# Performance work log

Hardware: AMD Instinct MI355X
Metric: run time of the kernel (lower is better)

## Reference

```python
import jax, jax.numpy as jnp
import numpy as np

N_NODES = 50000
N_EDGES = 800000
IN_DIM = 128
HID_DIM = 128
OUT_DIM = 128
NUM_GRAPHS = 64
NUM_CLASSES = 3


def _glorot(key, shape):
    lim = np.sqrt(6.0 / (shape[0] + shape[1])).astype(np.float32)
    return jax.random.uniform(key, shape, jnp.float32, -lim, lim)


def setup_inputs() -> dict:
    key = jax.random.key(0)
    ks = jax.random.split(key, 10)
    x = jax.random.normal(ks[0], (N_NODES, IN_DIM), jnp.float32)
    edge_index = jax.random.randint(ks[1], (2, N_EDGES), 0, N_NODES, jnp.int32).astype(jnp.int64)
    batch = jnp.sort(jax.random.randint(ks[2], (N_NODES,), 0, NUM_GRAPHS, jnp.int32)).astype(jnp.int64)
    return {
        "x": x,
        "edge_index": edge_index,
        "batch": batch,
        "W1": _glorot(ks[3], (IN_DIM, HID_DIM)),  "b1": jnp.zeros((HID_DIM,), jnp.float32),
        "W2": _glorot(ks[4], (HID_DIM, HID_DIM)), "b2": jnp.zeros((HID_DIM,), jnp.float32),
        "W3": _glorot(ks[5], (HID_DIM, OUT_DIM)), "b3": jnp.zeros((OUT_DIM,), jnp.float32),
        "C1": _glorot(ks[6], (OUT_DIM, HID_DIM)), "bc1": jnp.zeros((HID_DIM,), jnp.float32),
        "C2": _glorot(ks[7], (HID_DIM, NUM_CLASSES)), "bc2": jnp.zeros((NUM_CLASSES,), jnp.float32),
    }


def _gcn_conv(x, src, dst, norm, W, b):
    # PyG GCNConv: linear transform, then normalized gather/scatter aggregation, then bias.
    h = x @ W                               # [N, F_out]
    msg = h[src] * norm[:, None]            # [E+N, F_out] irregular gather
    return jax.ops.segment_sum(msg, dst, num_segments=N_NODES) + b


def reference(x, edge_index, batch, W1, b1, W2, b2, W3, b3, C1, bc1, C2, bc2):
    loops = jnp.arange(N_NODES, dtype=edge_index.dtype)
    src = jnp.concatenate([edge_index[0], loops])  # add self-loops as in GCNConv
    dst = jnp.concatenate([edge_index[1], loops])
    deg = jax.ops.segment_sum(jnp.ones_like(dst, jnp.float32), dst, num_segments=N_NODES)
    dinv = jnp.where(deg > 0, jax.lax.rsqrt(deg), 0.0)
    norm = dinv[src] * dinv[dst]            # symmetric D^-1/2 (A+I) D^-1/2 weights

    # dropout(p=0.2) is identity at inference time
    h = jax.nn.relu(_gcn_conv(x, src, dst, norm, W1, b1))
    h = jax.nn.relu(_gcn_conv(h, src, dst, norm, W2, b2))
    h = _gcn_conv(h, src, dst, norm, W3, b3)

    # global mean pool over batch segment ids
    counts = jax.ops.segment_sum(jnp.ones((N_NODES,), jnp.float32), batch, num_segments=NUM_GRAPHS)
    pooled = jax.ops.segment_sum(h, batch, num_segments=NUM_GRAPHS) / jnp.maximum(counts, 1.0)[:, None]

    g = jax.nn.relu(pooled @ C1 + bc1)      # classifier MLP (dropout 0.3 inactive)
    return g @ C2 + bc2                     # [NUM_GRAPHS, 3]
```

## Files before the change

kernel.cpp:

```cpp
#include <hip/hip_runtime.h>
#include <hip/hip_bf16.h>

#define N_NODES    50000
#define DIM        128
#define NUM_GRAPHS 64
#define NUM_CLASSES 3
#define NPAD       50176
#define XPITCH     136

typedef unsigned short ushort_t;
typedef unsigned int   uint_t;
typedef __attribute__((ext_vector_type(8))) short short8;
typedef __attribute__((ext_vector_type(4))) float f32x4;

__device__ __forceinline__ ushort_t f2bf(float f) {
    union { float f; uint_t u; } v; v.f = f;
    uint_t r = v.u + 0x7fffu + ((v.u >> 16) & 1u);
    return (ushort_t)(r >> 16);
}
__device__ __forceinline__ float bflo(uint_t u) {
    union { uint_t u; float f; } v; v.u = u << 16; return v.f;
}
__device__ __forceinline__ float bfhi(uint_t u) {
    union { uint_t u; float f; } v; v.u = u & 0xffff0000u; return v.f;
}

__device__ __forceinline__ void accum8(float* a, uint4 u) {
    a[0] += bflo(u.x); a[1] += bfhi(u.x);
    a[2] += bflo(u.y); a[3] += bfhi(u.y);
    a[4] += bflo(u.z); a[5] += bfhi(u.z);
    a[6] += bflo(u.w); a[7] += bfhi(u.w);
}

__device__ __forceinline__ int qsel(int lane, int s0, int s1, int s2, int s3) {
    int lo = (lane & 16) ? s1 : s0;
    int hi = (lane & 16) ? s3 : s2;
    return (lane & 32) ? hi : lo;
}

__device__ __forceinline__ void quad_gather(
    int lane, int m, int myidx0, int p0, int p1,
    const int* __restrict__ csr_src, const uint4* __restrict__ Tb4,
    float* a)
{
    int deg = p1 - p0;
    if (deg < 0) deg = 0;
    int nchunk = (deg + 63) >> 6;
    int myidx = myidx0;
    for (int ck = 0; ck < nchunk; ++ck) {
        int base = p0 + (ck << 6);
        int cnt = p1 - base; if (cnt > 64) cnt = 64;
        int nb = cnt >> 3;
        if (nb > 0) {
            uint4 u0, u1;
            {
                int s = qsel(lane, __builtin_amdgcn_readlane(myidx, 0),
                                   __builtin_amdgcn_readlane(myidx, 1),
                                   __builtin_amdgcn_readlane(myidx, 2),
                                   __builtin_amdgcn_readlane(myidx, 3));
                u0 = Tb4[s * 16 + m];
                s = qsel(lane, __builtin_amdgcn_readlane(myidx, 4),
                               __builtin_amdgcn_readlane(myidx, 5),
                               __builtin_amdgcn_readlane(myidx, 6),
                               __builtin_amdgcn_readlane(myidx, 7));
                u1 = Tb4[s * 16 + m];
            }
            for (int b = 1; b < nb; ++b) {
                int jb = b * 8;
                uint4 n0, n1;
                int s = qsel(lane, __builtin_amdgcn_readlane(myidx, jb),
                                   __builtin_amdgcn_readlane(myidx, jb + 1),
                                   __builtin_amdgcn_readlane(myidx, jb + 2),
                                   __builtin_amdgcn_readlane(myidx, jb + 3));
                n0 = Tb4[s * 16 + m];
                s = qsel(lane, __builtin_amdgcn_readlane(myidx, jb + 4),
                               __builtin_amdgcn_readlane(myidx, jb + 5),
                               __builtin_amdgcn_readlane(myidx, jb + 6),
                               __builtin_amdgcn_readlane(myidx, jb + 7));
                n1 = Tb4[s * 16 + m];
                accum8(a, u0); accum8(a, u1);
                u0 = n0; u1 = n1;
            }
            accum8(a, u0); accum8(a, u1);
        }
        int j = nb * 8;
        for (; j + 4 <= cnt; j += 4) {
            int s = qsel(lane, __builtin_amdgcn_readlane(myidx, j),
                               __builtin_amdgcn_readlane(myidx, j + 1),
                               __builtin_amdgcn_readlane(myidx, j + 2),
                               __builtin_amdgcn_readlane(myidx, j + 3));
            uint4 u = Tb4[s * 16 + m];
            accum8(a, u);
        }
        if (j < cnt) {
            int rem = cnt - j;
            int s0 = __builtin_amdgcn_readlane(myidx, j);
            int s1 = __builtin_amdgcn_readlane(myidx, (j + 1 < cnt) ? j + 1 : j);
            int s2 = __builtin_amdgcn_readlane(myidx, (j + 2 < cnt) ? j + 2 : j);
            int s  = qsel(lane, s0, s1, s2, s0);
            if ((lane >> 4) < rem) {
                uint4 u = Tb4[s * 16 + m];
                accum8(a, u);
            }
        }
        if (ck + 1 < nchunk) {
            int c2 = p1 - (base + 64);
            myidx = (lane < c2) ? csr_src[base + 64 + lane] : 0;
        }
    }
}

__global__ void k_init(int* degi, float* pooled, float* counts) {
    int i = blockIdx.x * 256 + threadIdx.x;
    if (i < NPAD) degi[i] = 0;
    if (i < NUM_GRAPHS * DIM) pooled[i] = 0.0f;
    if (i < NUM_GRAPHS) counts[i] = 0.0f;
}

__global__ void k_prep(const float* __restrict__ W1, const float* __restrict__ W2,
                       const float* __restrict__ W3, ushort_t* __restrict__ Wt) {
    int i = blockIdx.x * 256 + threadIdx.x;
    int mat = i >> 14;
    int idx = i & 16383;
    const float* W = (mat == 0) ? W1 : (mat == 1) ? W2 : W3;
    int n = idx >> 7, k = idx & 127;
    Wt[mat * 16384 + n * 128 + k] = f2bf(W[k * 128 + n]);
}

__global__ void k_count(const int* __restrict__ dst, int* degi, int* rank, int nedges) {
    int e = blockIdx.x * 256 + threadIdx.x;
    if (e < nedges) rank[e] = atomicAdd(&degi[dst[e]], 1);
}

__global__ __launch_bounds__(256) void k_scan1(const int* __restrict__ degi,
                                               int* rowptr, int* bsum) {
    __shared__ int sh[256];
    int i = blockIdx.x * 256 + threadIdx.x;
    int v = degi[i];
    sh[threadIdx.x] = v;
    __syncthreads();
    for (int off = 1; off < 256; off <<= 1) {
        int t = (threadIdx.x >= off) ? sh[threadIdx.x - off] : 0;
        __syncthreads();
        sh[threadIdx.x] += t;
        __syncthreads();
    }
    rowptr[i] = sh[threadIdx.x] - v;
    if (threadIdx.x == 255) bsum[blockIdx.x] = sh[255];
}

__global__ __launch_bounds__(256) void k_scan2(int* bsum, int nblocks) {
    __shared__ int sh[256];
    int v = (threadIdx.x < nblocks) ? bsum[threadIdx.x] : 0;
    sh[threadIdx.x] = v;
    __syncthreads();
    for (int off = 1; off < 256; off <<= 1) {
        int t = (threadIdx.x >= off) ? sh[threadIdx.x - off] : 0;
        __syncthreads();
        sh[threadIdx.x] += t;
        __syncthreads();
    }
    if (threadIdx.x < nblocks) bsum[threadIdx.x] = sh[threadIdx.x] - v;
}

__global__ __launch_bounds__(256) void k_scan3(int* rowptr, const int* __restrict__ bsum,
                                               const int* __restrict__ degi,
                                               float* dinv) {
    int i = blockIdx.x * 256 + threadIdx.x;
    rowptr[i] = rowptr[i] + bsum[blockIdx.x];
    if (i < N_NODES) dinv[i] = rsqrtf((float)degi[i] + 1.0f);
}

__global__ void k_fill(const int* __restrict__ src, const int* __restrict__ dst,
                       const int* __restrict__ rank, const int* __restrict__ rowptr,
                       int* csr_src, int nedges) {
    int e = blockIdx.x * 256 + threadIdx.x;
    if (e < nedges) csr_src[rowptr[dst[e]] + rank[e]] = src[e];
}

__global__ __launch_bounds__(256) void k_mm1(
    const float* __restrict__ xin, const ushort_t* __restrict__ WtG,
    const float* __restrict__ dinv, ushort_t* __restrict__ TbOut)
{
    __shared__ ushort_t Wl[DIM * XPITCH];
    __shared__ ushort_t Xl[64 * XPITCH];

    const int tid = threadIdx.x;
    const int rowbase = blockIdx.x * 64;

    #pragma unroll
    for (int i = 0; i < 8; ++i) {
        int g = tid + i * 256;
        uint4 v = ((const uint4*)WtG)[g];
        *((uint4*)&Wl[(g >> 4) * XPITCH + (g & 15) * 8]) = v;
    }
    #pragma unroll
    for (int i = 0; i < 8; ++i) {
        int c = tid + i * 256;
        int row = c >> 5;
        int grow = rowbase + row;
        float4 f = make_float4(0.f, 0.f, 0.f, 0.f);
        if (grow < N_NODES)
            f = ((const float4*)xin)[(long long)rowbase * 32 + c];
        ushort4 h;
        h.x = f2bf(f.x); h.y = f2bf(f.y); h.z = f2bf(f.z); h.w = f2bf(f.w);
        *((ushort4*)&Xl[row * XPITCH + (c & 31) * 4]) = h;
    }
    __syncthreads();

    const int wave = tid >> 6;
    const int lane = tid & 63;
    const int quad = lane >> 4;
    const int lm   = lane & 15;
    const int m0   = wave * 16;

    short8 af[4];
    #pragma unroll
    for (int k0 = 0; k0 < 4; ++k0)
        af[k0] = *(const short8*)&Xl[(m0 + lm) * XPITCH + k0 * 32 + quad * 8];

    int noder[4]; float di[4]; bool okr[4];
    #pragma unroll
    for (int r = 0; r < 4; ++r) {
        noder[r] = rowbase + m0 + quad * 4 + r;
        okr[r] = (noder[r] < N_NODES);
        di[r] = okr[r] ? dinv[noder[r]] : 0.f;
    }

    for (int n0 = 0; n0 < DIM; n0 += 16) {
        f32x4 acc = {0.f, 0.f, 0.f, 0.f};
        #pragma unroll
        for (int k0 = 0; k0 < 4; ++k0) {
            short8 bf = *(const short8*)&Wl[(n0 + lm) * XPITCH + k0 * 32 + quad * 8];
            acc = __builtin_amdgcn_mfma_f32_16x16x32_bf16(af[k0], bf, acc, 0, 0, 0);
        }
        int n = n0 + lm;
        #pragma unroll
        for (int r = 0; r < 4; ++r)
            if (okr[r])
                TbOut[(long long)noder[r] * DIM + n] = f2bf(acc[r] * di[r]);
    }
}

__global__ __launch_bounds__(256) void k_fused(
    const int* __restrict__ rowptr, const int* __restrict__ csr_src,
    const float* __restrict__ dinv, const uint_t* __restrict__ TbIn,
    const ushort_t* __restrict__ WtG, const float* __restrict__ b_prev,
    ushort_t* __restrict__ TbOut)
{
    __shared__ ushort_t Xl[16 * XPITCH];

    const int tid = threadIdx.x;
    const int rowbase = blockIdx.x * 16;
    const int wave = tid >> 6;
    const int lane = tid & 63;
    const int m    = lane & 15;
    const uint4* Tb4 = (const uint4*)TbIn;

    float4 blo = ((const float4*)b_prev)[m * 2];
    float4 bhi = ((const float4*)b_prev)[m * 2 + 1];

    const int nfirst = rowbase + wave * 4;
    int pv = (lane < 5) ? rowptr[nfirst + lane] : 0;
    int p[5];
    #pragma unroll
    for (int i = 0; i < 5; ++i) p[i] = __builtin_amdgcn_readlane(pv, i);

    int idx_n;
    {
        int d0 = p[1] - p[0];
        idx_n = (lane < d0) ? csr_src[p[0] + lane] : 0;
    }

    #pragma unroll
    for (int t = 0; t < 4; ++t) {
        int idx_cur = idx_n;
        if (t < 3) {
            int dn = p[t + 2] - p[t + 1];
            idx_n = (lane < dn) ? csr_src[p[t + 1] + lane] : 0;
        }
        int r = wave * 4 + t;
        int n = rowbase + r;
        float a[8] = {0.f, 0.f, 0.f, 0.f, 0.f, 0.f, 0.f, 0.f};
        float dd = 0.f;
        uint4 us = make_uint4(0u, 0u, 0u, 0u);
        if (n < N_NODES) {
            us = Tb4[n * 16 + m];
            dd = dinv[n];
            quad_gather(lane, m, idx_cur, p[t], p[t + 1], csr_src, Tb4, a);
        }
        #pragma unroll
        for (int i = 0; i < 8; ++i) {
            a[i] += __shfl_xor(a[i], 16);
            a[i] += __shfl_xor(a[i], 32);
        }
        accum8(a, us);
        if (lane < 16) {
            short8 hh;
            hh[0] = (short)f2bf(fmaxf(blo.x + a[0] * dd, 0.f));
            hh[1] = (short)f2bf(fmaxf(blo.y + a[1] * dd, 0.f));
            hh[2] = (short)f2bf(fmaxf(blo.z + a[2] * dd, 0.f));
            hh[3] = (short)f2bf(fmaxf(blo.w + a[3] * dd, 0.f));
            hh[4] = (short)f2bf(fmaxf(bhi.x + a[4] * dd, 0.f));
            hh[5] = (short)f2bf(fmaxf(bhi.y + a[5] * dd, 0.f));
            hh[6] = (short)f2bf(fmaxf(bhi.z + a[6] * dd, 0.f));
            hh[7] = (short)f2bf(fmaxf(bhi.w + a[7] * dd, 0.f));
            *((short8*)&Xl[r * XPITCH + m * 8]) = hh;
        }
    }
    __syncthreads();

    const int quad = lane >> 4;
    const int lm   = lane & 15;

    short8 af[4];
    #pragma unroll
    for (int k0 = 0; k0 < 4; ++k0)
        af[k0] = *(const short8*)&Xl[lm * XPITCH + k0 * 32 + quad * 8];

    int noder[4]; float di[4]; bool okr[4];
    #pragma unroll
    for (int r = 0; r < 4; ++r) {
        noder[r] = rowbase + quad * 4 + r;
        okr[r] = (noder[r] < N_NODES);
        di[r] = okr[r] ? dinv[noder[r]] : 0.f;
    }

    #pragma unroll
    for (int hh = 0; hh < 2; ++hh) {
        int n0 = wave * 32 + hh * 16;
        f32x4 acc = {0.f, 0.f, 0.f, 0.f};
        #pragma unroll
        for (int k0 = 0; k0 < 4; ++k0) {
            short8 bf = *(const short8*)&WtG[(n0 + lm) * DIM + k0 * 32 + quad * 8];
            acc = __builtin_amdgcn_mfma_f32_16x16x32_bf16(af[k0], bf, acc, 0, 0, 0);
        }
        int n = n0 + lm;
        #pragma unroll
        for (int r = 0; r < 4; ++r)
            if (okr[r])
                TbOut[(long long)noder[r] * DIM + n] = f2bf(acc[r] * di[r]);
    }
}

__global__ __launch_bounds__(256) void k_poolgather(
    const int* __restrict__ rowptr, const int* __restrict__ csr_src,
    const float* __restrict__ dinv, const uint_t* __restrict__ Tb,
    const float* __restrict__ b3, const int* __restrict__ batch,
    float* pooled, float* counts)
{
    __shared__ float lp[8][DIM];
    __shared__ float lc[8];

    const int tid  = threadIdx.x;
    const int wave = tid >> 6;
    const int lane = tid & 63;
    const int m    = lane & 15;
    const int q    = lane >> 4;
    const int blk0 = blockIdx.x * 32;
    const uint4* Tb4 = (const uint4*)Tb;
    const int ch = 8 * m + 2 * q;

    #pragma unroll
    for (int i = 0; i < 4; ++i) ((float*)lp)[tid + i * 256] = 0.f;
    if (tid < 8) lc[tid] = 0.f;
    __syncthreads();

    const int gbase = batch[min(blk0, N_NODES - 1)];
    int n0 = blk0 + wave * 8;

    if (n0 < N_NODES) {
        int nend = min(n0 + 8, N_NODES);
        float bb0 = b3[ch], bb1 = b3[ch + 1];

        int pv = (lane < 9) ? rowptr[min(n0 + lane, NPAD)] : 0;
        int p[9];
        #pragma unroll
        for (int i = 0; i < 9; ++i) p[i] = __builtin_amdgcn_readlane(pv, i);

        int cur = batch[n0];
        int runstart = n0;
        float2 pacc = make_float2(0.f, 0.f);

        int idx_n;
        {
            int d0 = p[1] - p[0];
            idx_n = (lane < d0) ? csr_src[p[0] + lane] : 0;
        }

        for (int i = 0; i < nend - n0; ++i) {
            int n = n0 + i;
            int idx_cur = idx_n;
            if (i < 7) {
                int dn = p[i + 2] - p[i + 1];
                idx_n = (lane < dn) ? csr_src[p[i + 1] + lane] : 0;
            }
            int g = batch[n];
            if (g != cur) {
                int slot = cur - gbase;
                if (slot < 8) {
                    atomicAdd(&lp[slot][ch], pacc.x);
                    atomicAdd(&lp[slot][ch + 1], pacc.y);
                    if (lane == 0) atomicAdd(&lc[slot], (float)(n - runstart));
                } else {
                    atomicAdd(&pooled[cur * DIM + ch], pacc.x);
                    atomicAdd(&pooled[cur * DIM + ch + 1], pacc.y);
                    if (lane == 0) atomicAdd(&counts[cur], (float)(n - runstart));
                }
                pacc.x = 0.f; pacc.y = 0.f; cur = g; runstart = n;
            }
            float a[8] = {0.f, 0.f, 0.f, 0.f, 0.f, 0.f, 0.f, 0.f};
            uint4 us = Tb4[n * 16 + m];
            quad_gather(lane, m, idx_cur, p[i], p[i + 1], csr_src, Tb4, a);
            #pragma unroll
            for (int k = 0; k < 8; ++k) {
                a[k] += __shfl_xor(a[k], 16);
                a[k] += __shfl_xor(a[k], 32);
            }
            accum8(a, us);
            float x0 = (q == 0) ? a[0] : (q == 1) ? a[2] : (q == 2) ? a[4] : a[6];
            float x1 = (q == 0) ? a[1] : (q == 1) ? a[3] : (q == 2) ? a[5] : a[7];
            float dd = dinv[n];
            pacc.x += bb0 + x0 * dd;
            pacc.y += bb1 + x1 * dd;
        }
        int slot = cur - gbase;
        if (slot < 8) {
            atomicAdd(&lp[slot][ch], pacc.x);
            atomicAdd(&lp[slot][ch + 1], pacc.y);
            if (lane == 0) atomicAdd(&lc[slot], (float)(nend - runstart));
        } else {
            atomicAdd(&pooled[cur * DIM + ch], pacc.x);
            atomicAdd(&pooled[cur * DIM + ch + 1], pacc.y);
            if (lane == 0) atomicAdd(&counts[cur], (float)(nend - runstart));
        }
    }
    __syncthreads();

    #pragma unroll
    for (int s = 0; s < 8; ++s) {
        if (lc[s] != 0.f) {
            if (tid < DIM) atomicAdd(&pooled[(gbase + s) * DIM + tid], lp[s][tid]);
            if (tid == DIM) atomicAdd(&counts[gbase + s], lc[s]);
        }
    }
}

__global__ __launch_bounds__(128) void k_cls(
    const float* __restrict__ pooled, const float* __restrict__ counts,
    const float* __restrict__ C1, const float* __restrict__ bc1,
    const float* __restrict__ C2, const float* __restrict__ bc2,
    float* out)
{
    __shared__ float pm[DIM];
    __shared__ float gv[DIM];
    int g = blockIdx.x, j = threadIdx.x;
    float cnt = fmaxf(counts[g], 1.0f);
    pm[j] = pooled[g * DIM + j] / cnt;
    __syncthreads();
    float a = bc1[j];
    for (int k = 0; k < DIM; ++k) a += pm[k] * C1[k * DIM + j];
    gv[j] = fmaxf(a, 0.f);
    __syncthreads();
    if (j < NUM_CLASSES) {
        float o = bc2[j];
        for (int k = 0; k < DIM; ++k) o += gv[k] * C2[k * NUM_CLASSES + j];
        out[g * NUM_CLASSES + j] = o;
    }
}

extern "C" void kernel_launch(void* const* d_in, const int* in_sizes, int n_in,
                              void* d_out, int out_size, void* d_ws, size_t ws_size,
                              hipStream_t stream) {
    const float* x    = (const float*)d_in[0];
    const int*   ei   = (const int*)d_in[1];
    const int*   batch= (const int*)d_in[2];
    const float* W1   = (const float*)d_in[3];
    const float* b1   = (const float*)d_in[4];
    const float* W2   = (const float*)d_in[5];
    const float* b2   = (const float*)d_in[6];
    const float* W3   = (const float*)d_in[7];
    const float* b3   = (const float*)d_in[8];
    const float* C1   = (const float*)d_in[9];
    const float* bc1  = (const float*)d_in[10];
    const float* C2   = (const float*)d_in[11];
    const float* bc2  = (const float*)d_in[12];

    const int nedges = in_sizes[1] / 2;
    const int* src = ei;
    const int* dst = ei + nedges;

    float*    dinv    = (float*)d_ws;
    uint_t*   TbA     = (uint_t*)(dinv + NPAD);
    uint_t*   TbB     = TbA + (long long)N_NODES * 64;
    float*    pooled  = (float*)(TbB + (long long)N_NODES * 64);
    float*    counts  = pooled + NUM_GRAPHS * DIM;
    int*      degi    = (int*)(counts + 64);
    int*      rowptr  = degi + NPAD;
    int*      bsum    = rowptr + NPAD + 256;
    int*      rank    = bsum + 256;
    int*      csr_src = rank + nedges;
    ushort_t* Wt      = (ushort_t*)(csr_src + nedges);

    const int nodeBlocks = NPAD / 256;
    const int mmBlocks   = (N_NODES + 63) / 64;
    const int fusedBlocks= (N_NODES + 15) / 16;
    const int pgBlocks   = (N_NODES + 31) / 32;
    const int edgeBlocks = (nedges + 255) / 256;

    k_init<<<nodeBlocks, 256, 0, stream>>>(degi, pooled, counts);
    k_prep<<<192, 256, 0, stream>>>(W1, W2, W3, Wt);
    k_count<<<edgeBlocks, 256, 0, stream>>>(dst, degi, rank, nedges);
    k_scan1<<<nodeBlocks, 256, 0, stream>>>(degi, rowptr, bsum);
    k_scan2<<<1, 256, 0, stream>>>(bsum, nodeBlocks);
    k_scan3<<<nodeBlocks, 256, 0, stream>>>(rowptr, bsum, degi, dinv);
    k_fill<<<edgeBlocks, 256, 0, stream>>>(src, dst, rank, rowptr, csr_src, nedges);

    k_mm1<<<mmBlocks, 256, 0, stream>>>(x, Wt, dinv, (ushort_t*)TbA);
    k_fused<<<fusedBlocks, 256, 0, stream>>>(rowptr, csr_src, dinv, TbA,
                                             Wt + 16384, b1, (ushort_t*)TbB);
    k_fused<<<fusedBlocks, 256, 0, stream>>>(rowptr, csr_src, dinv, TbB,
                                             Wt + 32768, b2, (ushort_t*)TbA);
    k_poolgather<<<pgBlocks, 256, 0, stream>>>(rowptr, csr_src, dinv, TbA,
                                               b3, batch, pooled, counts);
    k_cls<<<NUM_GRAPHS, 128, 0, stream>>>(pooled, counts, C1, bc1, C2, bc2,
                                          (float*)d_out);
}
```

Measured before the change: 285.6 us.

## Move dinv scaling into gather weights and fuse first matmul with degree counting

The source-side dinv scaling moves out of the matmul epilogues and into the gather loop, where each neighbor row is multiplied by its dinv read via readlane. With that dependency gone, the first matmul no longer needs dinv, so it runs in the same launch as the edge-degree counting (extra blocks do the atomics), and init and weight prep merge into one kernel. This cuts launches and lets the layer-1 GEMM overlap with the atomic histogram. The cost is an extra dinv gather per neighbor chunk and a multiply per accumulate in the hot gather loop.

```diff
diff --git a/kernel.cpp b/kernel.cpp
--- a/kernel.cpp
+++ b/kernel.cpp
@@ -7,6 +7,7 @@
 #define NUM_CLASSES 3
 #define NPAD       50176
 #define XPITCH     136
+#define MMB        782
 
 typedef unsigned short ushort_t;
 typedef unsigned int   uint_t;
@@ -24,12 +25,17 @@
 __device__ __forceinline__ float bfhi(uint_t u) {
     union { uint_t u; float f; } v; v.u = u & 0xffff0000u; return v.f;
 }
-
-__device__ __forceinline__ void accum8(float* a, uint4 u) {
-    a[0] += bflo(u.x); a[1] += bfhi(u.x);
-    a[2] += bflo(u.y); a[3] += bfhi(u.y);
-    a[4] += bflo(u.z); a[5] += bfhi(u.z);
-    a[6] += bflo(u.w); a[7] += bfhi(u.w);
+__device__ __forceinline__ float rlf(float v, int l) {
+    union { float f; int i; } c; c.f = v;
+    union { int i; float f; } d; d.i = __builtin_amdgcn_readlane(c.i, l);
+    return d.f;
+}
+
+__device__ __forceinline__ void wfma8(float* a, uint4 u, float w) {
+    a[0] += w * bflo(u.x); a[1] += w * bfhi(u.x);
+    a[2] += w * bflo(u.y); a[3] += w * bfhi(u.y);
+    a[4] += w * bflo(u.z); a[5] += w * bfhi(u.z);
+    a[6] += w * bflo(u.w); a[7] += w * bfhi(u.w);
 }
 
 __device__ __forceinline__ int qsel(int lane, int s0, int s1, int s2, int s3) {
@@ -37,51 +43,61 @@
     int hi = (lane & 16) ? s3 : s2;
     return (lane & 32) ? hi : lo;
 }
-
-__device__ __forceinline__ void quad_gather(
-    int lane, int m, int myidx0, int p0, int p1,
-    const int* __restrict__ csr_src, const uint4* __restrict__ Tb4,
-    float* a)
+__device__ __forceinline__ float qself(int lane, float s0, float s1, float s2, float s3) {
+    float lo = (lane & 16) ? s1 : s0;
+    float hi = (lane & 16) ? s3 : s2;
+    return (lane & 32) ? hi : lo;
+}
+
+__device__ __forceinline__ void quad_gather_w(
+    int lane, int m, int myidx0, float myw0, int p0, int p1,
+    const int* __restrict__ csr_src, const float* __restrict__ dinv,
+    const uint4* __restrict__ Tb4, float* a)
 {
     int deg = p1 - p0;
     if (deg < 0) deg = 0;
     int nchunk = (deg + 63) >> 6;
-    int myidx = myidx0;
+    int myidx = myidx0; float myw = myw0;
     for (int ck = 0; ck < nchunk; ++ck) {
         int base = p0 + (ck << 6);
         int cnt = p1 - base; if (cnt > 64) cnt = 64;
         int nb = cnt >> 3;
         if (nb > 0) {
-            uint4 u0, u1;
+            uint4 u0, u1; float w0, w1;
             {
                 int s = qsel(lane, __builtin_amdgcn_readlane(myidx, 0),
                                    __builtin_amdgcn_readlane(myidx, 1),
                                    __builtin_amdgcn_readlane(myidx, 2),
                                    __builtin_amdgcn_readlane(myidx, 3));
+                w0 = qself(lane, rlf(myw, 0), rlf(myw, 1), rlf(myw, 2), rlf(myw, 3));
                 u0 = Tb4[s * 16 + m];
                 s = qsel(lane, __builtin_amdgcn_readlane(myidx, 4),
                                __builtin_amdgcn_readlane(myidx, 5),
                                __builtin_amdgcn_readlane(myidx, 6),
                                __builtin_amdgcn_readlane(myidx, 7));
+                w1 = qself(lane, rlf(myw, 4), rlf(myw, 5), rlf(myw, 6), rlf(myw, 7));
                 u1 = Tb4[s * 16 + m];
             }
             for (int b = 1; b < nb; ++b) {
                 int jb = b * 8;
-                uint4 n0, n1;
                 int s = qsel(lane, __builtin_amdgcn_readlane(myidx, jb),
                                    __builtin_amdgcn_readlane(myidx, jb + 1),
                                    __builtin_amdgcn_readlane(myidx, jb + 2),
                                    __builtin_amdgcn_readlane(myidx, jb + 3));
-                n0 = Tb4[s * 16 + m];
+                float nw0 = qself(lane, rlf(myw, jb), rlf(myw, jb + 1),
+                                        rlf(myw, jb + 2), rlf(myw, jb + 3));
+                uint4 n0v = Tb4[s * 16 + m];
                 s = qsel(lane, __builtin_amdgcn_readlane(myidx, jb + 4),
                                __builtin_amdgcn_readlane(myidx, jb + 5),
                                __builtin_amdgcn_readlane(myidx, jb + 6),
                                __builtin_amdgcn_readlane(myidx, jb + 7));
-                n1 = Tb4[s * 16 + m];
-                accum8(a, u0); accum8(a, u1);
-                u0 = n0; u1 = n1;
+                float nw1 = qself(lane, rlf(myw, jb + 4), rlf(myw, jb + 5),
+                                        rlf(myw, jb + 6), rlf(myw, jb + 7));
+                uint4 n1v = Tb4[s * 16 + m];
+                wfma8(a, u0, w0); wfma8(a, u1, w1);
+                u0 = n0v; u1 = n1v; w0 = nw0; w1 = nw1;
             }
-            accum8(a, u0); accum8(a, u1);
+            wfma8(a, u0, w0); wfma8(a, u1, w1);
         }
         int j = nb * 8;
         for (; j + 4 <= cnt; j += 4) {
@@ -89,47 +105,47 @@
                                __builtin_amdgcn_readlane(myidx, j + 1),
                                __builtin_amdgcn_readlane(myidx, j + 2),
                                __builtin_amdgcn_readlane(myidx, j + 3));
+            float w = qself(lane, rlf(myw, j), rlf(myw, j + 1),
+                                  rlf(myw, j + 2), rlf(myw, j + 3));
             uint4 u = Tb4[s * 16 + m];
-            accum8(a, u);
+            wfma8(a, u, w);
         }
         if (j < cnt) {
             int rem = cnt - j;
-            int s0 = __builtin_amdgcn_readlane(myidx, j);
-            int s1 = __builtin_amdgcn_readlane(myidx, (j + 1 < cnt) ? j + 1 : j);
-            int s2 = __builtin_amdgcn_readlane(myidx, (j + 2 < cnt) ? j + 2 : j);
-            int s  = qsel(lane, s0, s1, s2, s0);
+            int j1 = (j + 1 < cnt) ? j + 1 : j;
+            int j2 = (j + 2 < cnt) ? j + 2 : j;
+            int s = qsel(lane, __builtin_amdgcn_readlane(myidx, j),
+                               __builtin_amdgcn_readlane(myidx, j1),
+                               __builtin_amdgcn_readlane(myidx, j2),
+                               __builtin_amdgcn_readlane(myidx, j));
+            float w = qself(lane, rlf(myw, j), rlf(myw, j1), rlf(myw, j2), rlf(myw, j));
             if ((lane >> 4) < rem) {
                 uint4 u = Tb4[s * 16 + m];
-                accum8(a, u);
+                wfma8(a, u, w);
             }
         }
         if (ck + 1 < nchunk) {
             int c2 = p1 - (base + 64);
             myidx = (lane < c2) ? csr_src[base + 64 + lane] : 0;
-        }
-    }
-}
-
-__global__ void k_init(int* degi, float* pooled, float* counts) {
+            myw = dinv[myidx];
+        }
+    }
+}
+
+__global__ void k_initprep(int* degi, float* pooled, float* counts,
+                           const float* __restrict__ W1, const float* __restrict__ W2,
+                           const float* __restrict__ W3, ushort_t* __restrict__ Wt) {
     int i = blockIdx.x * 256 + threadIdx.x;
     if (i < NPAD) degi[i] = 0;
     if (i < NUM_GRAPHS * DIM) pooled[i] = 0.0f;
     if (i < NUM_GRAPHS) counts[i] = 0.0f;
-}
-
-__global__ void k_prep(const float* __restrict__ W1, const float* __restrict__ W2,
-                       const float* __restrict__ W3, ushort_t* __restrict__ Wt) {
-    int i = blockIdx.x * 256 + threadIdx.x;
-    int mat = i >> 14;
-    int idx = i & 16383;
-    const float* W = (mat == 0) ? W1 : (mat == 1) ? W2 : W3;
-    int n = idx >> 7, k = idx & 127;
-    Wt[mat * 16384 + n * 128 + k] = f2bf(W[k * 128 + n]);
-}
-
-__global__ void k_count(const int* __restrict__ dst, int* degi, int* rank, int nedges) {
-    int e = blockIdx.x * 256 + threadIdx.x;
-    if (e < nedges) rank[e] = atomicAdd(&degi[dst[e]], 1);
+    if (i < 3 * 16384) {
+        int mat = i >> 14;
+        int idx = i & 16383;
+        const float* W = (mat == 0) ? W1 : (mat == 1) ? W2 : W3;
+        int n = idx >> 7, k = idx & 127;
+        Wt[mat * 16384 + n * 128 + k] = f2bf(W[k * 128 + n]);
+    }
 }
 
 __global__ __launch_bounds__(256) void k_scan1(const int* __restrict__ degi,
@@ -168,7 +184,7 @@
                                                float* dinv) {
     int i = blockIdx.x * 256 + threadIdx.x;
     rowptr[i] = rowptr[i] + bsum[blockIdx.x];
-    if (i < N_NODES) dinv[i] = rsqrtf((float)degi[i] + 1.0f);
+    dinv[i] = rsqrtf((float)degi[i] + 1.0f);
 }
 
 __global__ void k_fill(const int* __restrict__ src, const int* __restrict__ dst,
@@ -178,12 +194,19 @@
     if (e < nedges) csr_src[rowptr[dst[e]] + rank[e]] = src[e];
 }
 
-__global__ __launch_bounds__(256) void k_mm1(
+__global__ __launch_bounds__(256) void k_mm1c(
     const float* __restrict__ xin, const ushort_t* __restrict__ WtG,
-    const float* __restrict__ dinv, ushort_t* __restrict__ TbOut)
+    ushort_t* __restrict__ TbOut,
+    const int* __restrict__ dst, int* degi, int* rank, int nedges)
 {
     __shared__ ushort_t Wl[DIM * XPITCH];
     __shared__ ushort_t Xl[64 * XPITCH];
+
+    if ((int)blockIdx.x >= MMB) {
+        int e = ((int)blockIdx.x - MMB) * 256 + threadIdx.x;
+        if (e < nedges) rank[e] = atomicAdd(&degi[dst[e]], 1);
+        return;
+    }
 
     const int tid = threadIdx.x;
     const int rowbase = blockIdx.x * 64;
@@ -219,12 +242,11 @@
     for (int k0 = 0; k0 < 4; ++k0)
         af[k0] = *(const short8*)&Xl[(m0 + lm) * XPITCH + k0 * 32 + quad * 8];
 
-    int noder[4]; float di[4]; bool okr[4];
+    int noder[4]; bool okr[4];
     #pragma unroll
     for (int r = 0; r < 4; ++r) {
         noder[r] = rowbase + m0 + quad * 4 + r;
         okr[r] = (noder[r] < N_NODES);
-        di[r] = okr[r] ? dinv[noder[r]] : 0.f;
     }
 
     for (int n0 = 0; n0 < DIM; n0 += 16) {
@@ -238,7 +260,7 @@
         #pragma unroll
         for (int r = 0; r < 4; ++r)
             if (okr[r])
-                TbOut[(long long)noder[r] * DIM + n] = f2bf(acc[r] * di[r]);
+                TbOut[(long long)noder[r] * DIM + n] = f2bf(acc[r]);
     }
 }
 
@@ -266,35 +288,39 @@
     #pragma unroll
     for (int i = 0; i < 5; ++i) p[i] = __builtin_amdgcn_readlane(pv, i);
 
-    int idx_n;
+    const float4 dv = *(const float4*)&dinv[nfirst];
+
+    int idx_n; float w_n;
     {
         int d0 = p[1] - p[0];
         idx_n = (lane < d0) ? csr_src[p[0] + lane] : 0;
     }
+    w_n = dinv[idx_n];
 
     #pragma unroll
     for (int t = 0; t < 4; ++t) {
-        int idx_cur = idx_n;
+        int idx_cur = idx_n; float w_cur = w_n;
         if (t < 3) {
             int dn = p[t + 2] - p[t + 1];
             idx_n = (lane < dn) ? csr_src[p[t + 1] + lane] : 0;
         }
         int r = wave * 4 + t;
         int n = rowbase + r;
+        float dd = (t == 0) ? dv.x : (t == 1) ? dv.y : (t == 2) ? dv.z : dv.w;
         float a[8] = {0.f, 0.f, 0.f, 0.f, 0.f, 0.f, 0.f, 0.f};
-        float dd = 0.f;
         uint4 us = make_uint4(0u, 0u, 0u, 0u);
         if (n < N_NODES) {
             us = Tb4[n * 16 + m];
-            dd = dinv[n];
-            quad_gather(lane, m, idx_cur, p[t], p[t + 1], csr_src, Tb4, a);
-        }
+            quad_gather_w(lane, m, idx_cur, w_cur, p[t], p[t + 1],
+                          csr_src, dinv, Tb4, a);
+        }
+        if (t < 3) w_n = dinv[idx_n];
         #pragma unroll
         for (int i = 0; i < 8; ++i) {
             a[i] += __shfl_xor(a[i], 16);
             a[i] += __shfl_xor(a[i], 32);
         }
-        accum8(a, us);
+        wfma8(a, us, dd);
         if (lane < 16) {
             short8 hh;
             hh[0] = (short)f2bf(fmaxf(blo.x + a[0] * dd, 0.f));
@@ -318,12 +344,11 @@
     for (int k0 = 0; k0 < 4; ++k0)
         af[k0] = *(const short8*)&Xl[lm * XPITCH + k0 * 32 + quad * 8];
 
-    int noder[4]; float di[4]; bool okr[4];
+    int noder[4]; bool okr[4];
     #pragma unroll
     for (int r = 0; r < 4; ++r) {
         noder[r] = rowbase + quad * 4 + r;
         okr[r] = (noder[r] < N_NODES);
-        di[r] = okr[r] ? dinv[noder[r]] : 0.f;
     }
 
     #pragma unroll
@@ -339,7 +364,7 @@
         #pragma unroll
         for (int r = 0; r < 4; ++r)
             if (okr[r])
-                TbOut[(long long)noder[r] * DIM + n] = f2bf(acc[r] * di[r]);
+                TbOut[(long long)noder[r] * DIM + n] = f2bf(acc[r]);
     }
 }
 
@@ -382,15 +407,16 @@
         int runstart = n0;
         float2 pacc = make_float2(0.f, 0.f);
 
-        int idx_n;
+        int idx_n; float w_n;
         {
             int d0 = p[1] - p[0];
             idx_n = (lane < d0) ? csr_src[p[0] + lane] : 0;
         }
+        w_n = dinv[idx_n];
 
         for (int i = 0; i < nend - n0; ++i) {
             int n = n0 + i;
-            int idx_cur = idx_n;
+            int idx_cur = idx_n; float w_cur = w_n;
             if (i < 7) {
                 int dn = p[i + 2] - p[i + 1];
                 idx_n = (lane < dn) ? csr_src[p[i + 1] + lane] : 0;
@@ -411,16 +437,18 @@
             }
             float a[8] = {0.f, 0.f, 0.f, 0.f, 0.f, 0.f, 0.f, 0.f};
             uint4 us = Tb4[n * 16 + m];
-            quad_gather(lane, m, idx_cur, p[i], p[i + 1], csr_src, Tb4, a);
+            quad_gather_w(lane, m, idx_cur, w_cur, p[i], p[i + 1],
+                          csr_src, dinv, Tb4, a);
+            if (i < 7) w_n = dinv[idx_n];
             #pragma unroll
             for (int k = 0; k < 8; ++k) {
                 a[k] += __shfl_xor(a[k], 16);
                 a[k] += __shfl_xor(a[k], 32);
             }
-            accum8(a, us);
+            float dd = dinv[n];
+            wfma8(a, us, dd);
             float x0 = (q == 0) ? a[0] : (q == 1) ? a[2] : (q == 2) ? a[4] : a[6];
             float x1 = (q == 0) ? a[1] : (q == 1) ? a[3] : (q == 2) ? a[5] : a[7];
-            float dd = dinv[n];
             pacc.x += bb0 + x0 * dd;
             pacc.y += bb1 + x1 * dd;
         }
@@ -503,20 +531,18 @@
     ushort_t* Wt      = (ushort_t*)(csr_src + nedges);
 
     const int nodeBlocks = NPAD / 256;
-    const int mmBlocks   = (N_NODES + 63) / 64;
     const int fusedBlocks= (N_NODES + 15) / 16;
     const int pgBlocks   = (N_NODES + 31) / 32;
     const int edgeBlocks = (nedges + 255) / 256;
 
-    k_init<<<nodeBlocks, 256, 0, stream>>>(degi, pooled, counts);
-    k_prep<<<192, 256, 0, stream>>>(W1, W2, W3, Wt);
-    k_count<<<edgeBlocks, 256, 0, stream>>>(dst, degi, rank, nedges);
+    k_initprep<<<nodeBlocks, 256, 0, stream>>>(degi, pooled, counts, W1, W2, W3, Wt);
+    k_mm1c<<<MMB + edgeBlocks, 256, 0, stream>>>(x, Wt, (ushort_t*)TbA,
+                                                 dst, degi, rank, nedges);
     k_scan1<<<nodeBlocks, 256, 0, stream>>>(degi, rowptr, bsum);
     k_scan2<<<1, 256, 0, stream>>>(bsum, nodeBlocks);
     k_scan3<<<nodeBlocks, 256, 0, stream>>>(rowptr, bsum, degi, dinv);
     k_fill<<<edgeBlocks, 256, 0, stream>>>(src, dst, rank, rowptr, csr_src, nedges);
 
-    k_mm1<<<mmBlocks, 256, 0, stream>>>(x, Wt, dinv, (ushort_t*)TbA);
     k_fused<<<fusedBlocks, 256, 0, stream>>>(rowptr, csr_src, dinv, TbA,
                                              Wt + 16384, b1, (ushort_t*)TbB);
     k_fused<<<fusedBlocks, 256, 0, stream>>>(rowptr, csr_src, dinv, TbB,
```

Measured after the change: 284.9 us. Within noise of the previous version (-0.3%).
